# Performance work log

Hardware: AMD Instinct MI355X
Metric: run time of the kernel (lower is better)

Reference implementation:

```python
import jax, jax.numpy as jnp
import numpy as np

EPS_NORM = 1e-12  # torch F.normalize eps


def _resize_bilinear_ac(x, H, W):
    # Bilinear resize with align_corners=True on NCHW tensor x.
    h, w = x.shape[-2], x.shape[-1]
    ys = jnp.linspace(0.0, h - 1.0, H)
    xs = jnp.linspace(0.0, w - 1.0, W)
    y0 = jnp.floor(ys).astype(jnp.int32); y1 = jnp.minimum(y0 + 1, h - 1)
    x0 = jnp.floor(xs).astype(jnp.int32); x1 = jnp.minimum(x0 + 1, w - 1)
    wy = (ys - y0).astype(x.dtype)[None, None, :, None]
    wx = (xs - x0).astype(x.dtype)
    rows = x[:, :, y0, :] * (1 - wy) + x[:, :, y1, :] * wy  # (B,C,H,w)
    return rows[:, :, :, x0] * (1 - wx) + rows[:, :, :, x1] * wx  # (B,C,H,W)


def _icc(p, b):
    # p: (b, 19, hw) row-stochastic over hw.
    # M[i, j] = KLDiv(input=p_i, target=p_j, batchmean) = (1/b) * sum p_j*(log p_j - p_i)
    # NOTE: original code passes probabilities (not log-probs) as KLDiv input; kept faithful.
    E = jnp.sum(p * jnp.log(p), axis=(0, 2))            # (19,) sum_b,k p log p
    G = jnp.einsum('bik,bjk->ij', p, p)                  # (19,19) sum_b,k p_i p_j
    M = (E[None, :] - G) / b
    sym = jnp.triu(M) + jnp.triu(M, 1).T                 # loop writes value for i<=j to both [i,j],[j,i]
    nrm = jnp.maximum(jnp.linalg.norm(sym, axis=1, keepdims=True), EPS_NORM)
    return sym / nrm                                     # F.normalize(dim=1)


def reference(s_out, t_out, t_logit, s_logit, conv_w, conv_b):
    T = 1.0  # temperature
    # --- pi_loss ---
    B, C, H, W = t_out.shape
    s1 = _resize_bilinear_ac(s_out, H, W)
    s1 = jnp.einsum('bchw,oc->bohw', s1, conv_w[:, :, 0, 0]) + conv_b[None, :, None, None]
    log_ps = jax.nn.log_softmax(s1 / T, axis=1)
    pt = jax.nn.softmax(t_out / T, axis=1)
    # torch KLDivLoss() default reduction='mean' (mean over ALL elements)
    pi_loss = jnp.mean(pt * (jnp.log(pt) - log_ps))
    # --- lo_loss ---
    b, n, h, w = s_logit.shape
    tl = _resize_bilinear_ac(t_logit, h, w)
    s = jax.nn.softmax(s_logit.reshape(b, n, h * w) / T, axis=2)
    t = jax.nn.softmax(tl.reshape(b, n, h * w) / T, axis=2)
    ICCS = _icc(s, b)
    ICCT = _icc(t, b)
    lo_loss = jnp.sum((ICCS - ICCT) ** 2)
    return pi_loss, lo_loss


def setup_inputs() -> dict:
    key = jax.random.key(0)
    k = jax.random.split(key, 6)
    return {
        's_out': jax.random.normal(k[0], (8, 128, 33, 33), jnp.float32),
        't_out': jax.random.normal(k[1], (8, 768, 65, 65), jnp.float32),
        't_logit': jax.random.normal(k[2], (8, 19, 65, 65), jnp.float32),
        's_logit': jax.random.normal(k[3], (8, 19, 129, 129), jnp.float32),
        'conv_w': jax.random.normal(k[4], (768, 128, 1, 1), jnp.float32) * 0.05,
        'conv_b': jax.random.normal(k[5], (768,), jnp.float32) * 0.05,
    }
```

## Files before the change

### kernel.cpp

```cpp
#include <hip/hip_runtime.h>
#include <math.h>

#define WS_E0   0
#define WS_E1   19
#define WS_G0   64
#define WS_G1   448
#define WS_Z    1152
#define WS_WBF  2048
#define WS_PART 51200

typedef __bf16 bf16x8 __attribute__((ext_vector_type(8)));
typedef float  f32x4  __attribute__((ext_vector_type(4)));
typedef const __attribute__((address_space(1))) unsigned int guint;
typedef       __attribute__((address_space(3))) unsigned int luint;

__global__ void k_init(const float* __restrict__ conv_w, float* __restrict__ ws,
                       float* __restrict__ out) {
    const int bx = blockIdx.x, tid = threadIdx.x;
    if (bx < 96) {
        __bf16* Wb = (__bf16*)(ws + WS_WBF);
        #pragma unroll
        for (int j = 0; j < 4; j++) {
            int idx = bx * 1024 + j * 256 + tid;
            Wb[idx] = (__bf16)conv_w[idx];
        }
    } else {
        for (int k = tid; k < 2048; k += 256) ws[k] = 0.f;
        if (tid < 2) out[tid] = 0.f;
    }
}

__device__ __forceinline__ float t_resized(const float* __restrict__ Trow, int k) {
    int y = k / 129, x = k - y * 129;
    int y0 = y >> 1, x0 = x >> 1;
    int y1 = y0 + (y & 1), x1 = x0 + (x & 1);
    float fy = 0.5f * (float)(y & 1), fx = 0.5f * (float)(x & 1);
    float v00 = Trow[y0 * 65 + x0], v01 = Trow[y0 * 65 + x1];
    float v10 = Trow[y1 * 65 + x0], v11 = Trow[y1 * 65 + x1];
    float r0 = v00 + fx * (v01 - v00);
    float r1 = v10 + fx * (v11 - v10);
    return r0 + fy * (r1 - r0);
}

__launch_bounds__(256, 3)
__global__ void k_main(const float* __restrict__ s_out, const float* __restrict__ t_out,
                       const float* __restrict__ conv_w, const float* __restrict__ bias,
                       const float* __restrict__ s_logit, const float* __restrict__ t_logit,
                       float* __restrict__ ws, float* __restrict__ out) {
    __shared__ __align__(16) char lds[50176];
    const int tid = threadIdx.x;
    const int bx  = blockIdx.x;

    if (bx >= 304 && bx < 2416) {
        const int idx     = bx - 304;
        const int quarter = idx & 3;
        const int bs      = idx >> 2;
        const int b       = bs / 66;
        const int strip   = bs - b * 66;
        const int px0     = strip * 64;

        __bf16* xs = (__bf16*)lds;

        {
            const float* Sb = s_out + b * 128 * 1089;
            #pragma unroll
            for (int ii = 0; ii < 32; ii++) {
                int id2 = tid + ii * 256;
                int c = id2 >> 6, px = id2 & 63;
                int hw = px0 + px;
                int h = hw / 65, w = hw - h * 65;
                int y0 = h >> 1, x0 = w >> 1;
                int y1 = y0 + (h & 1), x1 = x0 + (w & 1);
                float wy = 0.5f * (float)(h & 1), wx = 0.5f * (float)(w & 1);
                const float* Sc = Sb + c * 1089;
                float v00 = Sc[y0 * 33 + x0], v01 = Sc[y0 * 33 + x1];
                float v10 = Sc[y1 * 33 + x0], v11 = Sc[y1 * 33 + x1];
                float r0 = v00 + wx * (v01 - v00);
                float r1 = v10 + wx * (v11 - v10);
                xs[px * 136 + c] = (__bf16)(r0 + wy * (r1 - r0));
            }
        }
        __syncthreads();

        const int l = tid & 63, g = tid >> 6, q = l >> 4, n = l & 15;
        const int m = n;

        bf16x8 bfrag[4][4];
        #pragma unroll
        for (int pt = 0; pt < 4; pt++)
            #pragma unroll
            for (int kf = 0; kf < 4; kf++)
                bfrag[pt][kf] = *(const bf16x8*)&xs[(pt * 16 + n) * 136 + kf * 32 + q * 8];

        const __bf16* Wbf = (const __bf16*)(ws + WS_WBF);
        const int og = quarter * 192 + g * 16;
        bf16x8 afr[3][4];
        f32x4  bq[3];
        #pragma unroll
        for (int c = 0; c < 3; c++) {
            const __bf16* Wr = Wbf + (size_t)(og + c * 64 + n) * 128 + q * 8;
            #pragma unroll
            for (int kf = 0; kf < 4; kf++) afr[c][kf] = *(const bf16x8*)(Wr + kf * 32);
            bq[c] = *(const f32x4*)&bias[og + c * 64 + q * 4];
        }

        const float* base_t = t_out + (size_t)(b * 768 + og) * 4225;
        int off[4];
        #pragma unroll
        for (int j = 0; j < 4; j++) {
            int col = ((m * 4) + j * 16) & 63;
            off[j] = (j * 4 + q) * 4225 + px0 + col;
        }
        int colr[4];
        #pragma unroll
        for (int pt = 0; pt < 4; pt++)
            colr[pt] = (((pt * 16 + (n & 12) - q * 16) & 63)) + (n & 3);

        char* lbw = lds + 17408 + g * 4096;
        auto issue_t = [&](int cc, int sel) {
            char* lb = lbw + sel * 16384;
            #pragma unroll
            for (int j = 0; j < 4; j++)
                __builtin_amdgcn_global_load_lds((guint*)(base_t + off[j] + cc * 270400),
                                                 (luint*)(lb + j * 1024), 16, 0, 0);
        };

        float Zt[4], St[4], Dd[4], Zs[4];
        #pragma unroll
        for (int pt = 0; pt < 4; pt++) { Zt[pt] = 0.f; St[pt] = 0.f; Dd[pt] = 0.f; Zs[pt] = 0.f; }

        issue_t(0, 0);
        #pragma unroll
        for (int c = 0; c < 3; c++) {
            const int cur = c & 1;
            if (c < 2) {
                issue_t(c + 1, 1 - cur);
                asm volatile("s_waitcnt vmcnt(4)" ::: "memory");
            } else {
                asm volatile("s_waitcnt vmcnt(0)" ::: "memory");
            }
            const float* tw = (const float*)(lbw + cur * 16384);
            #pragma unroll
            for (int pt = 0; pt < 4; pt++) {
                f32x4 a0 = {0.f, 0.f, 0.f, 0.f};
                #pragma unroll
                for (int kf = 0; kf < 4; kf++)
                    a0 = __builtin_amdgcn_mfma_f32_16x16x32_bf16(afr[c][kf], bfrag[pt][kf], a0, 0, 0, 0);
                #pragma unroll
                for (int r = 0; r < 4; r++) {
                    float tv  = tw[(q * 4 + r) * 64 + colr[pt]];
                    float s1v = a0[r] + bq[c][r];
                    float e   = __expf(tv);
                    Zt[pt] += e;
                    St[pt]  = fmaf(e, tv,  St[pt]);
                    Dd[pt]  = fmaf(e, s1v, Dd[pt]);
                    Zs[pt] += __expf(s1v);
                }
            }
        }

        __syncthreads();
        float* scr = (float*)lds;
        {
            int p = g * 4 + q;
            #pragma unroll
            for (int pt = 0; pt < 4; pt++) {
                f32x4 v = {Zt[pt], St[pt], Dd[pt], Zs[pt]};
                *(f32x4*)&scr[(pt * 16 + n) * 68 + p * 4] = v;
            }
        }
        __syncthreads();
        if (tid < 64) {
            float Z = 0.f, S = 0.f, D = 0.f, Z2 = 0.f;
            #pragma unroll
            for (int p = 0; p < 16; p++) {
                f32x4 v = *(const f32x4*)&scr[tid * 68 + p * 4];
                Z += v[0]; S += v[1]; D += v[2]; Z2 += v[3];
            }
            f32x4 o4 = {Z, S, D, Z2};
            *(f32x4*)&ws[WS_PART + (((size_t)quarter * 8 + b) * 4224 + px0 + tid) * 4] = o4;
        }
    } else if (bx < 304) {
        float* red = (float*)lds;
        int row  = bx;
        int side = (row >= 152) ? 1 : 0;
        int r    = side ? row - 152 : row;
        const float* src = side ? (t_logit + r * 4225) : (s_logit + r * 16641);

        float z = 0.f, s = 0.f;
        for (int k = tid; k < 16641; k += 256) {
            float v = side ? t_resized(src, k) : src[k];
            float e = __expf(v);
            z += e;
            s = fmaf(e, v, s);
        }
        for (int off = 32; off > 0; off >>= 1) { z += __shfl_down(z, off); s += __shfl_down(s, off); }
        if ((tid & 63) == 0) { red[tid >> 6] = z; red[4 + (tid >> 6)] = s; }
        __syncthreads();
        if (tid == 0) {
            float Z = red[0] + red[1] + red[2] + red[3];
            float S = red[4] + red[5] + red[6] + red[7];
            ws[WS_Z + row] = Z;
            atomicAdd(&ws[(side ? WS_E1 : WS_E0) + (r % 19)], S / Z - logf(Z));
        }
    } else {
        float* xc  = (float*)lds;
        float* red = (float*)lds + 128;
        const int b = bx - 2416;
        if (tid < 128) xc[tid] = s_out[((size_t)b * 128 + tid) * 1089 + 1088];
        __syncthreads();
        float z = 0.f, s = 0.f, d = 0.f, z2 = 0.f;
        #pragma unroll
        for (int rep = 0; rep < 3; rep++) {
            int o = tid + rep * 256;
            const float* Wr = conv_w + (size_t)o * 128;
            float s1 = bias[o];
            for (int cc = 0; cc < 128; cc++) s1 = fmaf(Wr[cc], xc[cc], s1);
            float tv = t_out[((size_t)(b * 768 + o)) * 4225 + 4224];
            float e  = __expf(tv);
            z += e; s = fmaf(e, tv, s); d = fmaf(e, s1, d); z2 += __expf(s1);
        }
        for (int off = 32; off > 0; off >>= 1) {
            z += __shfl_down(z, off); s += __shfl_down(s, off);
            d += __shfl_down(d, off); z2 += __shfl_down(z2, off);
        }
        if ((tid & 63) == 0) {
            int wv = tid >> 6;
            red[wv] = z; red[4 + wv] = s; red[8 + wv] = d; red[12 + wv] = z2;
        }
        __syncthreads();
        if (tid == 0) {
            float Z = red[0] + red[1] + red[2] + red[3];
            float S = red[4] + red[5] + red[6] + red[7];
            float D = red[8] + red[9] + red[10] + red[11];
            float Z2 = red[12] + red[13] + red[14] + red[15];
            float contrib = (S - D) / Z - logf(Z) + logf(Z2);
            atomicAdd(out, contrib * (1.0f / 25958400.0f));
        }
    }
}

#define KT 512
#define KP 516
__global__ void k_mid(const float* __restrict__ s_logit, const float* __restrict__ t_logit,
                      float* __restrict__ ws, float* __restrict__ out) {
    __shared__ __align__(16) char lds[39296];
    const int tid = threadIdx.x;
    const int bx  = blockIdx.x;

    if (bx < 528) {
        float* pbuf  = (float*)lds;
        float* rowiz = (float*)(lds + 39216);
        int side = (bx >= 264) ? 1 : 0;
        int rm   = side ? bx - 264 : bx;
        int b = rm / 33, kt = rm - b * 33;
        int k0 = kt * KT;

        if (tid < 19) rowiz[tid] = 1.0f / ws[WS_Z + side * 152 + b * 19 + tid];
        __syncthreads();

        for (int i = 0; i < 19; i++) {
            const float* src = side ? (t_logit + (b * 19 + i) * 4225) : (s_logit + (b * 19 + i) * 16641);
            float iz = rowiz[i];
            for (int kl = tid; kl < KT; kl += 256) {
                int k = k0 + kl;
                float p = 0.f;
                if (k < 16641) {
                    float v = side ? t_resized(src, k) : src[k];
                    p = __expf(v) * iz;
                }
                pbuf[i * KP + kl] = p;
            }
        }
        __syncthreads();

        if (tid < 190) {
            int t = tid, i = 0;
            while (t >= 19 - i) { t -= 19 - i; i++; }
            int j = i + t;
            const float* pi_ = &pbuf[i * KP];
            const float* pj_ = &pbuf[j * KP];
            float g = 0.f;
            #pragma unroll 4
            for (int kl = 0; kl < KT; kl += 4) {
                float4 a = *(const float4*)&pi_[kl];
                float4 c = *(const float4*)&pj_[kl];
                g = fmaf(a.x, c.x, g); g = fmaf(a.y, c.y, g);
                g = fmaf(a.z, c.z, g); g = fmaf(a.w, c.w, g);
            }
            atomicAdd(&ws[(side ? WS_G1 : WS_G0) + i * 19 + j], g);
        }
    } else {
        float* red = (float*)lds;
        int gp = (bx - 528) * 256 + tid;
        int b  = gp / 4224;
        int tp = gp - b * 4224;
        float Z = 0.f, S = 0.f, D = 0.f, Z2 = 0.f;
        #pragma unroll
        for (int qq = 0; qq < 4; qq++) {
            f32x4 v = *(const f32x4*)&ws[WS_PART + (((size_t)qq * 8 + b) * 4224 + tp) * 4];
            Z += v[0]; S += v[1]; D += v[2]; Z2 += v[3];
        }
        float contrib = (S - D) / Z - logf(Z) + logf(Z2);
        for (int off = 32; off > 0; off >>= 1) contrib += __shfl_down(contrib, off);
        if ((tid & 63) == 0) red[tid >> 6] = contrib;
        __syncthreads();
        if (tid == 0)
            atomicAdd(out, (red[0] + red[1] + red[2] + red[3]) * (1.0f / 25958400.0f));
    }
}

__global__ void k_final(const float* __restrict__ ws, float* __restrict__ out) {
    __shared__ float Ms[361], Mt[361], ns[19], nt[19];
    __shared__ float red[8];
    int tid = threadIdx.x;
    if (tid < 361) {
        int i = tid / 19, j = tid - i * 19;
        int lo = min(i, j), hi = max(i, j);
        Ms[tid] = (ws[WS_E0 + hi] - ws[WS_G0 + lo * 19 + hi]) * 0.125f;
        Mt[tid] = (ws[WS_E1 + hi] - ws[WS_G1 + lo * 19 + hi]) * 0.125f;
    }
    __syncthreads();
    if (tid < 19) {
        float as = 0.f, at = 0.f;
        for (int j = 0; j < 19; j++) {
            as = fmaf(Ms[tid * 19 + j], Ms[tid * 19 + j], as);
            at = fmaf(Mt[tid * 19 + j], Mt[tid * 19 + j], at);
        }
        ns[tid] = fmaxf(sqrtf(as), 1e-12f);
        nt[tid] = fmaxf(sqrtf(at), 1e-12f);
    }
    __syncthreads();
    float d = 0.f;
    if (tid < 361) {
        int i = tid / 19;
        float v = Ms[tid] / ns[i] - Mt[tid] / nt[i];
        d = v * v;
    }
    for (int off = 32; off > 0; off >>= 1) d += __shfl_down(d, off);
    if ((tid & 63) == 0) red[tid >> 6] = d;
    __syncthreads();
    if (tid == 0) out[1] = red[0] + red[1] + red[2] + red[3] + red[4] + red[5];
}

extern "C" void kernel_launch(void* const* d_in, const int* in_sizes, int n_in,
                              void* d_out, int out_size, void* d_ws, size_t ws_size,
                              hipStream_t stream) {
    const float* s_out   = (const float*)d_in[0];
    const float* t_out   = (const float*)d_in[1];
    const float* t_logit = (const float*)d_in[2];
    const float* s_logit = (const float*)d_in[3];
    const float* conv_w  = (const float*)d_in[4];
    const float* conv_b  = (const float*)d_in[5];
    float* out = (float*)d_out;
    float* ws  = (float*)d_ws;

    k_init<<<dim3(97), dim3(256), 0, stream>>>(conv_w, ws, out);
    k_main<<<dim3(2424), dim3(256), 0, stream>>>(s_out, t_out, conv_w, conv_b,
                                                 s_logit, t_logit, ws, out);
    k_mid<<<dim3(660), dim3(256), 0, stream>>>(s_logit, t_logit, ws, out);
    k_final<<<dim3(1), dim3(384), 0, stream>>>(ws, out);
}
```

Measured before the change: 245.8 us.

## Prefetch t_out tiles before resize phase and split dot accumulators

The main fused block now issues async global-to-LDS loads for t_out channel groups 0 and 1 before the bilinear resize of s_out. The third group goes into the freed xs region once the B fragments are in registers, so all three t tiles have their own buffers and no double-buffer reuse is needed. Weight fragment loads for the third group are deferred into the loop. Separately, the Gram dot-product loop uses four independent accumulators and some loops get unroll pragmas. The aim is to hide t_out load latency behind the resize and to shorten FMA dependency chains, at the cost of more LDS aliasing and an extra barrier.

```diff
diff --git a/kernel.cpp b/kernel.cpp
--- a/kernel.cpp
+++ b/kernel.cpp
@@ -58,6 +58,33 @@
         const int b       = bs / 66;
         const int strip   = bs - b * 66;
         const int px0     = strip * 64;
+
+        const int l = tid & 63, g = tid >> 6, q = l >> 4, n = l & 15;
+        const int og = quarter * 192 + g * 16;
+
+        const float* base_t = t_out + (size_t)(b * 768 + og) * 4225;
+        int off[4];
+        #pragma unroll
+        for (int j = 0; j < 4; j++) {
+            int col = ((n * 4) + j * 16) & 63;
+            off[j] = (j * 4 + q) * 4225 + px0 + col;
+        }
+        int colr[4];
+        #pragma unroll
+        for (int pt = 0; pt < 4; pt++)
+            colr[pt] = (((pt * 16 + (n & 12) - q * 16) & 63)) + (n & 3);
+
+        auto issue_t = [&](int cc) {
+            char* lb = (cc == 2) ? (lds + g * 4096) : (lds + 17408 + cc * 16384 + g * 4096);
+            const float* gb = base_t + (size_t)cc * 64 * 4225;
+            #pragma unroll
+            for (int j = 0; j < 4; j++)
+                __builtin_amdgcn_global_load_lds((guint*)(gb + off[j]),
+                                                 (luint*)(lb + j * 1024), 16, 0, 0);
+        };
+
+        issue_t(0);
+        issue_t(1);
 
         __bf16* xs = (__bf16*)lds;
 
@@ -80,10 +107,9 @@
                 xs[px * 136 + c] = (__bf16)(r0 + wy * (r1 - r0));
             }
         }
-        __syncthreads();
-
-        const int l = tid & 63, g = tid >> 6, q = l >> 4, n = l & 15;
-        const int m = n;
+        asm volatile("s_waitcnt lgkmcnt(0)" ::: "memory");
+        __builtin_amdgcn_s_barrier();
+        __builtin_amdgcn_sched_barrier(0);
 
         bf16x8 bfrag[4][4];
         #pragma unroll
@@ -93,53 +119,35 @@
                 bfrag[pt][kf] = *(const bf16x8*)&xs[(pt * 16 + n) * 136 + kf * 32 + q * 8];
 
         const __bf16* Wbf = (const __bf16*)(ws + WS_WBF);
-        const int og = quarter * 192 + g * 16;
         bf16x8 afr[3][4];
         f32x4  bq[3];
+        auto load_a = [&](int cc) {
+            const __bf16* Wr = Wbf + (size_t)(og + cc * 64 + n) * 128 + q * 8;
+            #pragma unroll
+            for (int kf = 0; kf < 4; kf++) afr[cc][kf] = *(const bf16x8*)(Wr + kf * 32);
+            bq[cc] = *(const f32x4*)&bias[og + cc * 64 + q * 4];
+        };
+        load_a(0);
+        load_a(1);
+
+        asm volatile("s_waitcnt lgkmcnt(0)" ::: "memory");
+        __builtin_amdgcn_s_barrier();
+        __builtin_amdgcn_sched_barrier(0);
+        issue_t(2);
+
+        float Zt[4], St[4], Dd[4], Zs[4];
+        #pragma unroll
+        for (int pt = 0; pt < 4; pt++) { Zt[pt] = 0.f; St[pt] = 0.f; Dd[pt] = 0.f; Zs[pt] = 0.f; }
+
         #pragma unroll
         for (int c = 0; c < 3; c++) {
-            const __bf16* Wr = Wbf + (size_t)(og + c * 64 + n) * 128 + q * 8;
-            #pragma unroll
-            for (int kf = 0; kf < 4; kf++) afr[c][kf] = *(const bf16x8*)(Wr + kf * 32);
-            bq[c] = *(const f32x4*)&bias[og + c * 64 + q * 4];
-        }
-
-        const float* base_t = t_out + (size_t)(b * 768 + og) * 4225;
-        int off[4];
-        #pragma unroll
-        for (int j = 0; j < 4; j++) {
-            int col = ((m * 4) + j * 16) & 63;
-            off[j] = (j * 4 + q) * 4225 + px0 + col;
-        }
-        int colr[4];
-        #pragma unroll
-        for (int pt = 0; pt < 4; pt++)
-            colr[pt] = (((pt * 16 + (n & 12) - q * 16) & 63)) + (n & 3);
-
-        char* lbw = lds + 17408 + g * 4096;
-        auto issue_t = [&](int cc, int sel) {
-            char* lb = lbw + sel * 16384;
-            #pragma unroll
-            for (int j = 0; j < 4; j++)
-                __builtin_amdgcn_global_load_lds((guint*)(base_t + off[j] + cc * 270400),
-                                                 (luint*)(lb + j * 1024), 16, 0, 0);
-        };
-
-        float Zt[4], St[4], Dd[4], Zs[4];
-        #pragma unroll
-        for (int pt = 0; pt < 4; pt++) { Zt[pt] = 0.f; St[pt] = 0.f; Dd[pt] = 0.f; Zs[pt] = 0.f; }
-
-        issue_t(0, 0);
-        #pragma unroll
-        for (int c = 0; c < 3; c++) {
-            const int cur = c & 1;
-            if (c < 2) {
-                issue_t(c + 1, 1 - cur);
-                asm volatile("s_waitcnt vmcnt(4)" ::: "memory");
-            } else {
-                asm volatile("s_waitcnt vmcnt(0)" ::: "memory");
-            }
-            const float* tw = (const float*)(lbw + cur * 16384);
+            if (c == 0)      asm volatile("s_waitcnt vmcnt(8)" ::: "memory");
+            else if (c == 1) asm volatile("s_waitcnt vmcnt(4)" ::: "memory");
+            else             asm volatile("s_waitcnt vmcnt(0)" ::: "memory");
+            if (c == 1) load_a(2);
+
+            const float* tw = (const float*)((c == 2) ? (lds + g * 4096)
+                                                      : (lds + 17408 + c * 16384 + g * 4096));
             #pragma unroll
             for (int pt = 0; pt < 4; pt++) {
                 f32x4 a0 = {0.f, 0.f, 0.f, 0.f};
@@ -188,6 +196,7 @@
         const float* src = side ? (t_logit + r * 4225) : (s_logit + r * 16641);
 
         float z = 0.f, s = 0.f;
+        #pragma unroll 4
         for (int k = tid; k < 16641; k += 256) {
             float v = side ? t_resized(src, k) : src[k];
             float e = __expf(v);
@@ -262,6 +271,7 @@
         for (int i = 0; i < 19; i++) {
             const float* src = side ? (t_logit + (b * 19 + i) * 4225) : (s_logit + (b * 19 + i) * 16641);
             float iz = rowiz[i];
+            #pragma unroll
             for (int kl = tid; kl < KT; kl += 256) {
                 int k = k0 + kl;
                 float p = 0.f;
@@ -280,15 +290,23 @@
             int j = i + t;
             const float* pi_ = &pbuf[i * KP];
             const float* pj_ = &pbuf[j * KP];
-            float g = 0.f;
-            #pragma unroll 4
-            for (int kl = 0; kl < KT; kl += 4) {
-                float4 a = *(const float4*)&pi_[kl];
-                float4 c = *(const float4*)&pj_[kl];
-                g = fmaf(a.x, c.x, g); g = fmaf(a.y, c.y, g);
-                g = fmaf(a.z, c.z, g); g = fmaf(a.w, c.w, g);
-            }
-            atomicAdd(&ws[(side ? WS_G1 : WS_G0) + i * 19 + j], g);
+            float g0 = 0.f, g1 = 0.f, g2 = 0.f, g3 = 0.f;
+            #pragma unroll 2
+            for (int kl = 0; kl < KT; kl += 16) {
+                float4 a0 = *(const float4*)&pi_[kl];      float4 c0 = *(const float4*)&pj_[kl];
+                float4 a1 = *(const float4*)&pi_[kl + 4];  float4 c1 = *(const float4*)&pj_[kl + 4];
+                float4 a2 = *(const float4*)&pi_[kl + 8];  float4 c2 = *(const float4*)&pj_[kl + 8];
+                float4 a3 = *(const float4*)&pi_[kl + 12]; float4 c3 = *(const float4*)&pj_[kl + 12];
+                g0 = fmaf(a0.x, c0.x, g0); g0 = fmaf(a0.y, c0.y, g0);
+                g0 = fmaf(a0.z, c0.z, g0); g0 = fmaf(a0.w, c0.w, g0);
+                g1 = fmaf(a1.x, c1.x, g1); g1 = fmaf(a1.y, c1.y, g1);
+                g1 = fmaf(a1.z, c1.z, g1); g1 = fmaf(a1.w, c1.w, g1);
+                g2 = fmaf(a2.x, c2.x, g2); g2 = fmaf(a2.y, c2.y, g2);
+                g2 = fmaf(a2.z, c2.z, g2); g2 = fmaf(a2.w, c2.w, g2);
+                g3 = fmaf(a3.x, c3.x, g3); g3 = fmaf(a3.y, c3.y, g3);
+                g3 = fmaf(a3.z, c3.z, g3); g3 = fmaf(a3.w, c3.w, g3);
+            }
+            atomicAdd(&ws[(side ? WS_G1 : WS_G0) + i * 19 + j], (g0 + g1) + (g2 + g3));
         }
     } else {
         float* red = (float*)lds;
```

Result: faster. 239.7 us (-2.5%).
